# Performance work log

Measured on AMD Instinct MI355X. Metric: run time of the kernel, lower is better.

## Reference

```python
import jax, jax.numpy as jnp
import numpy as np

EPS = 0.5
MIN_SAMPLES = 5


def setup_inputs() -> dict:
    key = jax.random.key(0)
    X = jax.random.uniform(key, (12288, 8), dtype=jnp.float32)
    return {"X": X}


def reference(X):
    """DBSCAN: eps-range queries + cluster expansion, expressed as
    eps-graph connected components over core points (same clustering
    as the serial BFS in the original module; cluster ids are assigned
    in order of each cluster's minimum core index, matching the
    ascending-scan discovery order of the original)."""
    N = X.shape[0]
    SENTINEL = jnp.int32(N)

    # pairwise squared Euclidean distances [N, N] (KDTree range query equivalent)
    sq = jnp.sum(X * X, axis=1)
    d2 = sq[:, None] + sq[None, :] - 2.0 * (X @ X.T)
    adj = d2 <= (EPS * EPS)                      # eps-neighborhood (includes self)

    density = jnp.sum(adj, axis=1)               # |query_ball_point(x_i, eps)|
    core = density >= MIN_SAMPLES                # core-point mask

    # core-core edges: BFS expansion only propagates through cores
    core_adj = adj & core[None, :] & core[:, None]

    idx = jnp.arange(N, dtype=jnp.int32)
    init = jnp.where(core, idx, SENTINEL)        # each core starts as its own root

    def prop(lbl):
        # min label over core neighbors (min-plus propagation = connected components)
        nb_min = jnp.min(jnp.where(core_adj, lbl[None, :], SENTINEL), axis=1)
        return jnp.minimum(lbl, nb_min)

    def cond(state):
        cur, prev = state
        return jnp.any(cur != prev)

    def body(state):
        cur, _ = state
        return prop(cur), cur

    lbl, _ = jax.lax.while_loop(cond, body, (prop(init), init))

    # border points: non-core points within eps of a core join that core's cluster
    core_nb = jnp.min(jnp.where(adj & core[None, :], lbl[None, :], SENTINEL), axis=1)
    root = jnp.where(core, lbl, core_nb)         # SENTINEL -> noise

    # compact cluster ids: rank of each cluster root (min core index) ascending,
    # matching the original's sequential discovery order k = 0, 1, ...
    is_root = core & (lbl == idx)
    rank = jnp.cumsum(is_root.astype(jnp.int32)) - 1   # rank[i] valid where is_root[i]
    labels = jnp.where(root < SENTINEL,
                       rank[jnp.clip(root, 0, N - 1)],
                       jnp.int32(-1))
    return labels
```

## Files before the change

kernel.cpp:

```cpp
#include <hip/hip_runtime.h>

#define NPTS 12288
#define DIMS 8
#define EPS2 0.25f
#define MINS 5
#define NIB1 (NPTS / 256)
#define NW   (NPTS / 32)
#define SENT NPTS
#define RMAX 512
#define W    (RMAX / 32)
#define BIGL 0x3fffffff
#define FT   128
#define FB   256
#define FBGRID 256
#define HB   96
#define HT   512

#define ATHR 256
#define AROWS 2
#define ATI  (ATHR * AROWS)
#define ANIB (NPTS / ATI)
#define ANJB 48
#define AJC  (NPTS / ANJB)
#define AWCH (AJC / 32)

typedef float v2f __attribute__((ext_vector_type(2)));

__device__ __forceinline__ float dot8(const v2f* xi, const float4& a, const float4& b) {
  v2f y0 = {a.x, a.y}, y1 = {a.z, a.w}, y2 = {b.x, b.y}, y3 = {b.z, b.w};
  v2f d = xi[0] * y0;
  d = __builtin_elementwise_fma(xi[1], y1, d);
  d = __builtin_elementwise_fma(xi[2], y2, d);
  d = __builtin_elementwise_fma(xi[3], y3, d);
  return d.x + d.y;
}


__global__ __launch_bounds__(ATHR) void k_adj(const float* __restrict__ X,
                                              unsigned int* __restrict__ adj,
                                              int* __restrict__ density) {
  __shared__ float4 xs[AJC][2];
  __shared__ float sqs[AJC];
  int t = threadIdx.x;
  int j0 = blockIdx.y * AJC;
  {
    int j = j0 + t;
    float4 a = ((const float4*)X)[j * 2];
    float4 b = ((const float4*)X)[j * 2 + 1];
    xs[t][0] = a; xs[t][1] = b;
    float sv = 0.f;
    sv = fmaf(a.x, a.x, sv); sv = fmaf(a.y, a.y, sv); sv = fmaf(a.z, a.z, sv); sv = fmaf(a.w, a.w, sv);
    sv = fmaf(b.x, b.x, sv); sv = fmaf(b.y, b.y, sv); sv = fmaf(b.z, b.z, sv); sv = fmaf(b.w, b.w, sv);
    sqs[t] = sv;
  }
  int i0 = blockIdx.x * ATI + t, i1 = i0 + ATHR;
  v2f xi0[4], xi1[4];
  {
    float4 a0 = ((const float4*)X)[i0 * 2], b0v = ((const float4*)X)[i0 * 2 + 1];
    float4 a1 = ((const float4*)X)[i1 * 2], b1v = ((const float4*)X)[i1 * 2 + 1];
    xi0[0] = (v2f){a0.x, a0.y}; xi0[1] = (v2f){a0.z, a0.w};
    xi0[2] = (v2f){b0v.x, b0v.y}; xi0[3] = (v2f){b0v.z, b0v.w};
    xi1[0] = (v2f){a1.x, a1.y}; xi1[1] = (v2f){a1.z, a1.w};
    xi1[2] = (v2f){b1v.x, b1v.y}; xi1[3] = (v2f){b1v.z, b1v.w};
  }
  float sq0 = 0.f, sq1 = 0.f;
#pragma unroll
  for (int q = 0; q < 4; q++) {
    v2f p0 = xi0[q] * xi0[q], p1 = xi1[q] * xi1[q];
    sq0 += p0.x + p0.y; sq1 += p1.x + p1.y;
  }
  __syncthreads();
  unsigned int acc0[AWCH], acc1[AWCH];
#pragma unroll
  for (int w = 0; w < AWCH; w++) {
    unsigned int b0 = 0u, b1 = 0u;
#pragma unroll 4
    for (int bit = 0; bit < 32; bit++) {
      int jj = (w << 5) + bit;
      float4 xa = xs[jj][0], xb = xs[jj][1];
      float sj = sqs[jj];
      unsigned int m = 1u << bit;
      float d20 = (sq0 + sj) - 2.0f * dot8(xi0, xa, xb);
      float d21 = (sq1 + sj) - 2.0f * dot8(xi1, xa, xb);
      if (d20 <= EPS2) b0 |= m;
      if (d21 <= EPS2) b1 |= m;
    }
    acc0[w] = b0; acc1[w] = b1;
  }
  uint4* dst0 = (uint4*)(adj + (size_t)i0 * NW + blockIdx.y * AWCH);
  uint4* dst1 = (uint4*)(adj + (size_t)i1 * NW + blockIdx.y * AWCH);
  dst0[0] = make_uint4(acc0[0], acc0[1], acc0[2], acc0[3]);
  dst0[1] = make_uint4(acc0[4], acc0[5], acc0[6], acc0[7]);
  dst1[0] = make_uint4(acc1[0], acc1[1], acc1[2], acc1[3]);
  dst1[1] = make_uint4(acc1[4], acc1[5], acc1[6], acc1[7]);
  int pc0 = 0, pc1 = 0;
#pragma unroll
  for (int w = 0; w < AWCH; w++) { pc0 += __popc(acc0[w]); pc1 += __popc(acc1[w]); }
  atomicAdd(&density[i0], pc0);
  atomicAdd(&density[i1], pc1);
}

__global__ __launch_bounds__(HT) void k_hook2(const unsigned int* __restrict__ adj,
                                              const int* __restrict__ density,
                                              unsigned long long* __restrict__ corebm,
                                              int* __restrict__ hook) {
  __shared__ unsigned long long cb64[NW / 2];
  const unsigned int* cb = (const unsigned int*)cb64;
  int t = threadIdx.x;
  for (int base = 0; base < NPTS; base += HT) {
    int i = base + t;
    unsigned long long m = __ballot(density[i] >= MINS);
    if ((t & 63) == 0) cb64[i >> 6] = m;
  }
  __syncthreads();
  if (blockIdx.x == 0) {
    for (int w = t; w < NW / 2; w += HT) corebm[w] = cb64[w];
  }
  int lane = t & 63, wv = t >> 6;
  int gw = blockIdx.x * (HT / 64) + wv;
  for (int i = gw; i < NPTS; i += (HT / 64) * HB) {
    const unsigned int* row = adj + (size_t)i * NW;
    int wi = i >> 5;
    int m = i;
    for (int w = lane; w <= wi; w += 64) {
      unsigned int x = row[w] & cb[w];
      if (w == wi) x &= (1u << (i & 31)) - 1;
      if (x) m = min(m, (w << 5) + __ffs(x) - 1);
    }
#pragma unroll
    for (int off = 32; off >= 1; off >>= 1) m = min(m, __shfl_xor(m, off, 64));
    if (lane == 0) hook[i] = m;
  }
}

__global__ __launch_bounds__(1024) void k_rid(const int* __restrict__ density,
                                              const int* __restrict__ hook,
                                              int* __restrict__ Rptr,
                                              int* __restrict__ labL,
                                              int* __restrict__ bcount) {
  __shared__ unsigned short ridS[NPTS];
  __shared__ int wsum[16];
  int t = threadIdx.x;
  int lane = t & 63, wid = t >> 6;
  const int SEG = NPTS / 1024;
  int base = t * SEG;
  int flags = 0;
  int s = 0;
#pragma unroll
  for (int k = 0; k < SEG; k++) {
    int i = base + k;
    int f = (density[i] >= MINS && hook[i] == i) ? 1 : 0;
    flags |= f << k;
    s += f;
  }
  int segsum = s;
#pragma unroll
  for (int off = 1; off < 64; off <<= 1) {
    int n = __shfl_up(s, off, 64);
    if (lane >= off) s += n;
  }
  if (lane == 63) wsum[wid] = s;
  __syncthreads();
  int woff = 0;
  for (int w = 0; w < wid; w++) woff += wsum[w];
  int run = woff + s - segsum;
#pragma unroll
  for (int k = 0; k < SEG; k++) {
    ridS[base + k] = (unsigned short)run;
    run += (flags >> k) & 1;
  }
  if (t == 1023) *Rptr = run;
  if (t == 0) *bcount = 0;
  __syncthreads();
  for (int k = 0; k < SEG; k++) {
    int i = base + k;
    int lab = -1;
    if (density[i] >= MINS) {
      int v = i, h = hook[v];
      while (h != v) { v = h; h = hook[v]; }
      lab = min((int)ridS[v], RMAX - 1);
    }
    labL[i] = lab;
  }
}

__global__ __launch_bounds__(FB) void k_fillbm(const unsigned int* __restrict__ adj,
                                               const unsigned int* __restrict__ cb32,
                                               const int* __restrict__ labL,
                                               unsigned int* __restrict__ bm) {
  __shared__ unsigned int bmL[RMAX * W];
  __shared__ unsigned short labS[NPTS];
  __shared__ unsigned int cb[NW];
  int t = threadIdx.x;
  for (int q = t; q < RMAX * W; q += FB) bmL[q] = 0u;
  for (int q = t; q < NPTS; q += FB) labS[q] = (unsigned short)(labL[q] + 1);
  for (int w = t; w < NW; w += FB) cb[w] = cb32[w];
  __syncthreads();
  int lane = t & 63, wv = t >> 6;
  int gw = blockIdx.x * 4 + wv;
  for (int i = gw; i < NPTS; i += 4 * FBGRID) {
    int a0 = (int)labS[i] - 1;
    if (a0 < 0) continue;
    const unsigned int* row = adj + (size_t)i * NW;
    int wi = i >> 5;
    for (int w = wi + lane; w < NW; w += 64) {
      unsigned int x = row[w] & cb[w];
      if (w == wi) x &= (0xFFFFFFFEu << (i & 31));
      while (x) {
        int b = __ffs(x) - 1; x &= x - 1;
        int lj = (int)labS[(w << 5) + b] - 1;
        if (lj != a0) {
          atomicOr(&bmL[a0 * W + (lj >> 5)], 1u << (lj & 31));
          atomicOr(&bmL[lj * W + (a0 >> 5)], 1u << (a0 & 31));
        }
      }
    }
  }
  __syncthreads();
  for (int q = t; q < RMAX * W; q += FB) {
    unsigned int v = bmL[q];
    if (v) atomicOr(&bm[q], v);
  }
}

__global__ __launch_bounds__(RMAX) void k_cc(const unsigned int* __restrict__ bm,
                                             const int* __restrict__ Rptr,
                                             const int* __restrict__ labL,
                                             int* __restrict__ labArr,
                                             int* __restrict__ blist,
                                             int* __restrict__ bcount,
                                             float* __restrict__ out) {
  __shared__ int lbl[RMAX];
  __shared__ int mn[RMAX];
  __shared__ int chg, cmp;
  int a = threadIdx.x;
  int R = *Rptr; if (R > RMAX) R = RMAX;
  lbl[a] = a;
  __syncthreads();
  while (true) {
    int m = lbl[a];
    if (a < R) {
      const unsigned int* row = bm + a * W;
#pragma unroll
      for (int w = 0; w < W; w++) {
        unsigned int bits = row[w];
        while (bits) {
          int b = __ffs(bits) - 1;
          bits &= bits - 1;
          m = min(m, lbl[(w << 5) + b]);
        }
      }
    }
    mn[a] = m;
    if (a == 0) chg = 0;
    __syncthreads();
    int l = lbl[a];
    if (m < l) { atomicMin(&lbl[l], m); atomicMin(&lbl[a], m); chg = 1; }
    __syncthreads();
    while (true) {
      if (a == 0) cmp = 0;
      __syncthreads();
      int nl = lbl[lbl[a]];
      __syncthreads();
      if (nl < lbl[a]) { lbl[a] = nl; cmp = 1; }
      __syncthreads();
      if (!cmp) break;
    }
    if (!chg) break;
    __syncthreads();
  }
  int flag = (a < R && lbl[a] == a) ? 1 : 0;
  mn[a] = flag;
  __syncthreads();
  for (int off = 1; off < RMAX; off <<= 1) {
    int v = mn[a];
    int add = (a >= off) ? mn[a - off] : 0;
    __syncthreads();
    mn[a] = v + add;
    __syncthreads();
  }
  int myclab = mn[lbl[a]] - 1;
  mn[a] = myclab;
  __syncthreads();
  for (int base = 0; base < NPTS; base += RMAX) {
    int i = base + a;
    int l = labL[i];
    if (l >= 0) {
      int lab = mn[l];
      labArr[i] = lab;
      out[i] = (float)lab;
    } else {
      labArr[i] = BIGL;
      out[i] = -1.0f;
      int pos = atomicAdd(bcount, 1);
      blist[pos] = i;
    }
  }
}

__global__ __launch_bounds__(FT) void k_border(const unsigned int* __restrict__ adj,
                                               const unsigned int* __restrict__ cb32,
                                               const int* __restrict__ labArr,
                                               const int* __restrict__ blist,
                                               const int* __restrict__ bcount,
                                               float* __restrict__ out) {
  __shared__ unsigned int cb[NW];
  __shared__ int wm[FT / 64];
  int t = threadIdx.x;
  for (int w = t; w < NW; w += FT) cb[w] = cb32[w];
  __syncthreads();
  int count = *bcount;
  for (int k = blockIdx.x; k < count; k += gridDim.x) {
    int p = blist[k];
    const unsigned int* row = adj + (size_t)p * NW;
    int m = BIGL;
    for (int w = t; w < NW; w += FT) {
      unsigned int x = row[w] & cb[w];
      while (x) {
        int b = __ffs(x) - 1; x &= x - 1;
        m = min(m, labArr[(w << 5) + b]);
      }
    }
#pragma unroll
    for (int off = 32; off >= 1; off >>= 1) m = min(m, __shfl_xor(m, off, 64));
    if ((t & 63) == 0) wm[t >> 6] = m;
    __syncthreads();
    if (t == 0) {
      int mm = min(wm[0], wm[1]);
      out[p] = (mm < BIGL) ? (float)mm : -1.0f;
    }
    __syncthreads();
  }
}


extern "C" void kernel_launch(void* const* d_in, const int* in_sizes, int n_in,
                              void* d_out, int out_size, void* d_ws, size_t ws_size,
                              hipStream_t stream) {
  const float* X = (const float*)d_in[0];
  float* out = (float*)d_out;

  char* ws = (char*)d_ws;
  unsigned int* adj = (unsigned int*)ws;
  size_t off = (size_t)NPTS * NW * 4;
  int* density = (int*)(ws + off);           off += 4 * NPTS;
  int* hook    = (int*)(ws + off);           off += 4 * NPTS;
  int* labL    = (int*)(ws + off);           off += 4 * NPTS;
  int* labArr  = (int*)(ws + off);           off += 4 * NPTS;
  int* blist   = (int*)(ws + off);           off += 4 * NPTS;
  unsigned long long* corebm = (unsigned long long*)(ws + off); off += 2048;
  unsigned int* bm  = (unsigned int*)(ws + off); off += 4 * RMAX * W;
  int* Rptr    = (int*)(ws + off);
  int* bcount  = Rptr + 1;

  hipMemsetAsync(density, 0, 4 * NPTS, stream);
  hipMemsetAsync(bm, 0, 4 * RMAX * W, stream);

  dim3 gridA(ANIB, ANJB);

  k_adj<<<gridA, ATHR, 0, stream>>>(X, adj, density);
  k_hook2<<<HB, HT, 0, stream>>>(adj, density, corebm, hook);
  k_rid<<<1, 1024, 0, stream>>>(density, hook, Rptr, labL, bcount);
  k_fillbm<<<FBGRID, FB, 0, stream>>>(adj, (const unsigned int*)corebm, labL, bm);
  k_cc<<<1, RMAX, 0, stream>>>(bm, Rptr, labL, labArr, blist, bcount, out);
  k_border<<<256, FT, 0, stream>>>(adj, (const unsigned int*)corebm, labArr, blist, bcount, out);
}
```

Before: 241.5 us.

## Fuse post-adjacency stages into one persistent kernel with software grid barriers

Replaces the five kernels after the adjacency build (hook, root id, bitmap fill, component merge, border assignment) with a single persistent 256-block kernel that separates phases with an atomic generation-counter grid barrier. Density is now computed from adjacency rows inside that kernel instead of with atomics in k_adj, and the two memsets shrink to one tiny control reset. The goal is to remove the launch gaps and tail idle time between many small kernels. In exchange, correctness depends on all 256 blocks being co-resident, and the single-block phases leave the rest of the grid spinning at barriers.

```diff
diff --git a/kernel.cpp b/kernel.cpp
--- a/kernel.cpp
+++ b/kernel.cpp
@@ -4,21 +4,17 @@
 #define DIMS 8
 #define EPS2 0.25f
 #define MINS 5
-#define NIB1 (NPTS / 256)
 #define NW   (NPTS / 32)
-#define SENT NPTS
 #define RMAX 512
 #define W    (RMAX / 32)
 #define BIGL 0x3fffffff
-#define FT   128
-#define FB   256
-#define FBGRID 256
-#define HB   96
-#define HT   512
+
+#define MB   256
+#define MT   512
+#define MW   (MB * MT / 64)
 
 #define ATHR 256
-#define AROWS 2
-#define ATI  (ATHR * AROWS)
+#define ATI  512
 #define ANIB (NPTS / ATI)
 #define ANJB 48
 #define AJC  (NPTS / ANJB)
@@ -35,10 +31,8 @@
   return d.x + d.y;
 }
 
-
 __global__ __launch_bounds__(ATHR) void k_adj(const float* __restrict__ X,
-                                              unsigned int* __restrict__ adj,
-                                              int* __restrict__ density) {
+                                              unsigned int* __restrict__ adj) {
   __shared__ float4 xs[AJC][2];
   __shared__ float sqs[AJC];
   int t = threadIdx.x;
@@ -93,243 +87,252 @@
   dst0[1] = make_uint4(acc0[4], acc0[5], acc0[6], acc0[7]);
   dst1[0] = make_uint4(acc1[0], acc1[1], acc1[2], acc1[3]);
   dst1[1] = make_uint4(acc1[4], acc1[5], acc1[6], acc1[7]);
-  int pc0 = 0, pc1 = 0;
-#pragma unroll
-  for (int w = 0; w < AWCH; w++) { pc0 += __popc(acc0[w]); pc1 += __popc(acc1[w]); }
-  atomicAdd(&density[i0], pc0);
-  atomicAdd(&density[i1], pc1);
-}
-
-__global__ __launch_bounds__(HT) void k_hook2(const unsigned int* __restrict__ adj,
-                                              const int* __restrict__ density,
-                                              unsigned long long* __restrict__ corebm,
-                                              int* __restrict__ hook) {
-  __shared__ unsigned long long cb64[NW / 2];
-  const unsigned int* cb = (const unsigned int*)cb64;
+}
+
+__device__ __forceinline__ void gridbar(int* cnt, int* gen, int t) {
+  __syncthreads();
+  __threadfence();
+  if (t == 0) {
+    int g = __hip_atomic_load(gen, __ATOMIC_RELAXED, __HIP_MEMORY_SCOPE_AGENT);
+    int v = __hip_atomic_fetch_add(cnt, 1, __ATOMIC_ACQ_REL, __HIP_MEMORY_SCOPE_AGENT);
+    if (v == MB - 1) {
+      __hip_atomic_store(cnt, 0, __ATOMIC_RELAXED, __HIP_MEMORY_SCOPE_AGENT);
+      __hip_atomic_fetch_add(gen, 1, __ATOMIC_ACQ_REL, __HIP_MEMORY_SCOPE_AGENT);
+    } else {
+      while (__hip_atomic_load(gen, __ATOMIC_ACQUIRE, __HIP_MEMORY_SCOPE_AGENT) == g)
+        __builtin_amdgcn_s_sleep(8);
+    }
+  }
+  __syncthreads();
+}
+
+__global__ __launch_bounds__(MT) void k_mega(const unsigned int* __restrict__ adj,
+                                             int* __restrict__ density,
+                                             int* __restrict__ hook,
+                                             int* __restrict__ labL,
+                                             int* __restrict__ labArr,
+                                             int* __restrict__ blist,
+                                             unsigned int* __restrict__ bm,
+                                             int* __restrict__ clabG,
+                                             int* __restrict__ Rptr,
+                                             int* __restrict__ cnt,
+                                             int* __restrict__ gen,
+                                             int* __restrict__ bcount,
+                                             float* __restrict__ out) {
+  __shared__ unsigned long long cb64S[NW / 2];
+  __shared__ unsigned int big[RMAX * W + NPTS / 2];
+  __shared__ int wsum[MT / 64];
+  __shared__ int chg, cmp;
+  unsigned int* cbS = (unsigned int*)cb64S;
   int t = threadIdx.x;
-  for (int base = 0; base < NPTS; base += HT) {
+  int lane = t & 63, wv = t >> 6;
+  int gw = blockIdx.x * (MT / 64) + wv;
+
+  if (blockIdx.x == 0)
+    for (int q = t; q < RMAX * W; q += MT) bm[q] = 0u;
+  for (int i = gw; i < NPTS; i += MW) {
+    const uint4* row = (const uint4*)(adj + (size_t)i * NW);
+    uint4 v = row[lane];
+    int s = __popc(v.x) + __popc(v.y) + __popc(v.z) + __popc(v.w);
+    if (lane < NW / 4 - 64) {
+      uint4 v2 = row[64 + lane];
+      s += __popc(v2.x) + __popc(v2.y) + __popc(v2.z) + __popc(v2.w);
+    }
+#pragma unroll
+    for (int off = 32; off >= 1; off >>= 1) s += __shfl_xor(s, off, 64);
+    if (lane == 0) density[i] = s;
+  }
+  gridbar(cnt, gen, t);
+
+  for (int base = 0; base < NPTS; base += MT) {
     int i = base + t;
     unsigned long long m = __ballot(density[i] >= MINS);
-    if ((t & 63) == 0) cb64[i >> 6] = m;
+    if ((t & 63) == 0) cb64S[i >> 6] = m;
   }
   __syncthreads();
-  if (blockIdx.x == 0) {
-    for (int w = t; w < NW / 2; w += HT) corebm[w] = cb64[w];
-  }
-  int lane = t & 63, wv = t >> 6;
-  int gw = blockIdx.x * (HT / 64) + wv;
-  for (int i = gw; i < NPTS; i += (HT / 64) * HB) {
+  for (int i = gw; i < NPTS; i += MW) {
     const unsigned int* row = adj + (size_t)i * NW;
     int wi = i >> 5;
     int m = i;
     for (int w = lane; w <= wi; w += 64) {
-      unsigned int x = row[w] & cb[w];
-      if (w == wi) x &= (1u << (i & 31)) - 1;
+      unsigned int x = row[w] & cbS[w];
+      if (w == wi) x &= (1u << (i & 31)) - 1u;
       if (x) m = min(m, (w << 5) + __ffs(x) - 1);
     }
 #pragma unroll
     for (int off = 32; off >= 1; off >>= 1) m = min(m, __shfl_xor(m, off, 64));
     if (lane == 0) hook[i] = m;
   }
-}
-
-__global__ __launch_bounds__(1024) void k_rid(const int* __restrict__ density,
-                                              const int* __restrict__ hook,
-                                              int* __restrict__ Rptr,
-                                              int* __restrict__ labL,
-                                              int* __restrict__ bcount) {
-  __shared__ unsigned short ridS[NPTS];
-  __shared__ int wsum[16];
-  int t = threadIdx.x;
-  int lane = t & 63, wid = t >> 6;
-  const int SEG = NPTS / 1024;
-  int base = t * SEG;
-  int flags = 0;
-  int s = 0;
-#pragma unroll
-  for (int k = 0; k < SEG; k++) {
-    int i = base + k;
-    int f = (density[i] >= MINS && hook[i] == i) ? 1 : 0;
-    flags |= f << k;
-    s += f;
-  }
-  int segsum = s;
-#pragma unroll
-  for (int off = 1; off < 64; off <<= 1) {
-    int n = __shfl_up(s, off, 64);
-    if (lane >= off) s += n;
-  }
-  if (lane == 63) wsum[wid] = s;
-  __syncthreads();
-  int woff = 0;
-  for (int w = 0; w < wid; w++) woff += wsum[w];
-  int run = woff + s - segsum;
-#pragma unroll
-  for (int k = 0; k < SEG; k++) {
-    ridS[base + k] = (unsigned short)run;
-    run += (flags >> k) & 1;
-  }
-  if (t == 1023) *Rptr = run;
-  if (t == 0) *bcount = 0;
-  __syncthreads();
-  for (int k = 0; k < SEG; k++) {
-    int i = base + k;
-    int lab = -1;
-    if (density[i] >= MINS) {
-      int v = i, h = hook[v];
-      while (h != v) { v = h; h = hook[v]; }
-      lab = min((int)ridS[v], RMAX - 1);
-    }
-    labL[i] = lab;
-  }
-}
-
-__global__ __launch_bounds__(FB) void k_fillbm(const unsigned int* __restrict__ adj,
-                                               const unsigned int* __restrict__ cb32,
-                                               const int* __restrict__ labL,
-                                               unsigned int* __restrict__ bm) {
-  __shared__ unsigned int bmL[RMAX * W];
-  __shared__ unsigned short labS[NPTS];
-  __shared__ unsigned int cb[NW];
-  int t = threadIdx.x;
-  for (int q = t; q < RMAX * W; q += FB) bmL[q] = 0u;
-  for (int q = t; q < NPTS; q += FB) labS[q] = (unsigned short)(labL[q] + 1);
-  for (int w = t; w < NW; w += FB) cb[w] = cb32[w];
-  __syncthreads();
-  int lane = t & 63, wv = t >> 6;
-  int gw = blockIdx.x * 4 + wv;
-  for (int i = gw; i < NPTS; i += 4 * FBGRID) {
-    int a0 = (int)labS[i] - 1;
-    if (a0 < 0) continue;
-    const unsigned int* row = adj + (size_t)i * NW;
-    int wi = i >> 5;
-    for (int w = wi + lane; w < NW; w += 64) {
-      unsigned int x = row[w] & cb[w];
-      if (w == wi) x &= (0xFFFFFFFEu << (i & 31));
-      while (x) {
-        int b = __ffs(x) - 1; x &= x - 1;
-        int lj = (int)labS[(w << 5) + b] - 1;
-        if (lj != a0) {
-          atomicOr(&bmL[a0 * W + (lj >> 5)], 1u << (lj & 31));
-          atomicOr(&bmL[lj * W + (a0 >> 5)], 1u << (a0 & 31));
+  gridbar(cnt, gen, t);
+
+  if (blockIdx.x == 0) {
+    unsigned short* ridS = (unsigned short*)big;
+    const int SEG = NPTS / MT;
+    int base = t * SEG;
+    int flags = 0, s = 0;
+    for (int k = 0; k < SEG; k++) {
+      int i = base + k;
+      int f = (density[i] >= MINS && hook[i] == i) ? 1 : 0;
+      flags |= f << k;
+      s += f;
+    }
+    int segsum = s;
+#pragma unroll
+    for (int off = 1; off < 64; off <<= 1) {
+      int n = __shfl_up(s, off, 64);
+      if (lane >= off) s += n;
+    }
+    if (lane == 63) wsum[wv] = s;
+    __syncthreads();
+    int woff = 0;
+    for (int w = 0; w < wv; w++) woff += wsum[w];
+    int run = woff + s - segsum;
+    for (int k = 0; k < SEG; k++) {
+      ridS[base + k] = (unsigned short)run;
+      run += (flags >> k) & 1;
+    }
+    if (t == MT - 1) *Rptr = run;
+    __syncthreads();
+    for (int k = 0; k < SEG; k++) {
+      int i = base + k;
+      int lab = -1;
+      if (density[i] >= MINS) {
+        int v = i, h = hook[v];
+        while (h != v) { v = h; h = hook[v]; }
+        lab = min((int)ridS[v], RMAX - 1);
+      }
+      labL[i] = lab;
+    }
+  }
+  gridbar(cnt, gen, t);
+
+  {
+    unsigned int* bmL = big;
+    unsigned short* labS = (unsigned short*)(big + RMAX * W);
+    for (int q = t; q < RMAX * W; q += MT) bmL[q] = 0u;
+    for (int q = t; q < NPTS; q += MT) labS[q] = (unsigned short)(labL[q] + 1);
+    __syncthreads();
+    for (int i = gw; i < NPTS; i += MW) {
+      int a0 = (int)labS[i] - 1;
+      if (a0 < 0) continue;
+      const unsigned int* row = adj + (size_t)i * NW;
+      int wi = i >> 5;
+      for (int w = wi + lane; w < NW; w += 64) {
+        unsigned int x = row[w] & cbS[w];
+        if (w == wi) x &= (0xFFFFFFFEu << (i & 31));
+        while (x) {
+          int b = __ffs(x) - 1; x &= x - 1;
+          int lj = (int)labS[(w << 5) + b] - 1;
+          if (lj != a0) {
+            atomicOr(&bmL[a0 * W + (lj >> 5)], 1u << (lj & 31));
+            atomicOr(&bmL[lj * W + (a0 >> 5)], 1u << (a0 & 31));
+          }
         }
       }
     }
-  }
-  __syncthreads();
-  for (int q = t; q < RMAX * W; q += FB) {
-    unsigned int v = bmL[q];
-    if (v) atomicOr(&bm[q], v);
-  }
-}
-
-__global__ __launch_bounds__(RMAX) void k_cc(const unsigned int* __restrict__ bm,
-                                             const int* __restrict__ Rptr,
-                                             const int* __restrict__ labL,
-                                             int* __restrict__ labArr,
-                                             int* __restrict__ blist,
-                                             int* __restrict__ bcount,
-                                             float* __restrict__ out) {
-  __shared__ int lbl[RMAX];
-  __shared__ int mn[RMAX];
-  __shared__ int chg, cmp;
-  int a = threadIdx.x;
-  int R = *Rptr; if (R > RMAX) R = RMAX;
-  lbl[a] = a;
-  __syncthreads();
-  while (true) {
-    int m = lbl[a];
-    if (a < R) {
-      const unsigned int* row = bm + a * W;
-#pragma unroll
-      for (int w = 0; w < W; w++) {
-        unsigned int bits = row[w];
-        while (bits) {
-          int b = __ffs(bits) - 1;
-          bits &= bits - 1;
-          m = min(m, lbl[(w << 5) + b]);
+    __syncthreads();
+    for (int q = t; q < RMAX * W; q += MT) {
+      unsigned int v = bmL[q];
+      if (v) atomicOr(&bm[q], v);
+    }
+  }
+  gridbar(cnt, gen, t);
+
+  if (blockIdx.x == 0) {
+    int* lbl = (int*)big;
+    int* mn = lbl + RMAX;
+    int a = t;
+    int R = *Rptr; if (R > RMAX) R = RMAX;
+    lbl[a] = a;
+    __syncthreads();
+    while (true) {
+      int m = lbl[a];
+      if (a < R) {
+        const unsigned int* row = bm + a * W;
+#pragma unroll
+        for (int w = 0; w < W; w++) {
+          unsigned int bits = row[w];
+          while (bits) {
+            int b = __ffs(bits) - 1;
+            bits &= bits - 1;
+            m = min(m, lbl[(w << 5) + b]);
+          }
         }
       }
-    }
-    mn[a] = m;
-    if (a == 0) chg = 0;
-    __syncthreads();
-    int l = lbl[a];
-    if (m < l) { atomicMin(&lbl[l], m); atomicMin(&lbl[a], m); chg = 1; }
-    __syncthreads();
-    while (true) {
-      if (a == 0) cmp = 0;
-      __syncthreads();
-      int nl = lbl[lbl[a]];
-      __syncthreads();
-      if (nl < lbl[a]) { lbl[a] = nl; cmp = 1; }
-      __syncthreads();
-      if (!cmp) break;
-    }
-    if (!chg) break;
-    __syncthreads();
-  }
-  int flag = (a < R && lbl[a] == a) ? 1 : 0;
-  mn[a] = flag;
-  __syncthreads();
-  for (int off = 1; off < RMAX; off <<= 1) {
-    int v = mn[a];
-    int add = (a >= off) ? mn[a - off] : 0;
-    __syncthreads();
-    mn[a] = v + add;
-    __syncthreads();
-  }
-  int myclab = mn[lbl[a]] - 1;
-  mn[a] = myclab;
-  __syncthreads();
-  for (int base = 0; base < NPTS; base += RMAX) {
-    int i = base + a;
-    int l = labL[i];
-    if (l >= 0) {
-      int lab = mn[l];
-      labArr[i] = lab;
-      out[i] = (float)lab;
-    } else {
-      labArr[i] = BIGL;
-      out[i] = -1.0f;
-      int pos = atomicAdd(bcount, 1);
-      blist[pos] = i;
-    }
-  }
-}
-
-__global__ __launch_bounds__(FT) void k_border(const unsigned int* __restrict__ adj,
-                                               const unsigned int* __restrict__ cb32,
-                                               const int* __restrict__ labArr,
-                                               const int* __restrict__ blist,
-                                               const int* __restrict__ bcount,
-                                               float* __restrict__ out) {
-  __shared__ unsigned int cb[NW];
-  __shared__ int wm[FT / 64];
-  int t = threadIdx.x;
-  for (int w = t; w < NW; w += FT) cb[w] = cb32[w];
-  __syncthreads();
-  int count = *bcount;
-  for (int k = blockIdx.x; k < count; k += gridDim.x) {
-    int p = blist[k];
-    const unsigned int* row = adj + (size_t)p * NW;
-    int m = BIGL;
-    for (int w = t; w < NW; w += FT) {
-      unsigned int x = row[w] & cb[w];
-      while (x) {
-        int b = __ffs(x) - 1; x &= x - 1;
-        m = min(m, labArr[(w << 5) + b]);
-      }
-    }
-#pragma unroll
-    for (int off = 32; off >= 1; off >>= 1) m = min(m, __shfl_xor(m, off, 64));
-    if ((t & 63) == 0) wm[t >> 6] = m;
-    __syncthreads();
-    if (t == 0) {
-      int mm = min(wm[0], wm[1]);
-      out[p] = (mm < BIGL) ? (float)mm : -1.0f;
-    }
-    __syncthreads();
+      mn[a] = m;
+      if (a == 0) chg = 0;
+      __syncthreads();
+      int l = lbl[a];
+      if (m < l) { atomicMin(&lbl[l], m); atomicMin(&lbl[a], m); chg = 1; }
+      __syncthreads();
+      while (true) {
+        if (a == 0) cmp = 0;
+        __syncthreads();
+        int nl = lbl[lbl[a]];
+        __syncthreads();
+        if (nl < lbl[a]) { lbl[a] = nl; cmp = 1; }
+        __syncthreads();
+        if (!cmp) break;
+      }
+      if (!chg) break;
+      __syncthreads();
+    }
+    int flag = (a < R && lbl[a] == a) ? 1 : 0;
+    mn[a] = flag;
+    __syncthreads();
+    for (int off = 1; off < RMAX; off <<= 1) {
+      int v = mn[a];
+      int add = (a >= off) ? mn[a - off] : 0;
+      __syncthreads();
+      mn[a] = v + add;
+      __syncthreads();
+    }
+    clabG[a] = mn[lbl[a]] - 1;
+  }
+  gridbar(cnt, gen, t);
+
+  {
+    int gid = blockIdx.x * MT + t;
+    if (gid < NPTS) {
+      int l = labL[gid];
+      if (l >= 0) {
+        int lab = clabG[l];
+        labArr[gid] = lab;
+        out[gid] = (float)lab;
+      } else {
+        labArr[gid] = BIGL;
+        out[gid] = -1.0f;
+        int pos = atomicAdd(bcount, 1);
+        blist[pos] = gid;
+      }
+    }
+  }
+  gridbar(cnt, gen, t);
+
+  {
+    int count = *bcount;
+    for (int k = blockIdx.x; k < count; k += MB) {
+      int p = blist[k];
+      const unsigned int* row = adj + (size_t)p * NW;
+      int m = BIGL;
+      if (t < NW) {
+        unsigned int x = row[t] & cbS[t];
+        while (x) {
+          int b = __ffs(x) - 1; x &= x - 1;
+          m = min(m, labArr[(t << 5) + b]);
+        }
+      }
+#pragma unroll
+      for (int off = 32; off >= 1; off >>= 1) m = min(m, __shfl_xor(m, off, 64));
+      if (lane == 0) wsum[wv] = m;
+      __syncthreads();
+      if (t == 0) {
+        int mm = wsum[0];
+        for (int w = 1; w < MT / 64; w++) mm = min(mm, wsum[w]);
+        out[p] = (mm < BIGL) ? (float)mm : -1.0f;
+      }
+      __syncthreads();
+    }
   }
 }
 
@@ -348,20 +351,17 @@
   int* labL    = (int*)(ws + off);           off += 4 * NPTS;
   int* labArr  = (int*)(ws + off);           off += 4 * NPTS;
   int* blist   = (int*)(ws + off);           off += 4 * NPTS;
-  unsigned long long* corebm = (unsigned long long*)(ws + off); off += 2048;
-  unsigned int* bm  = (unsigned int*)(ws + off); off += 4 * RMAX * W;
-  int* Rptr    = (int*)(ws + off);
-  int* bcount  = Rptr + 1;
-
-  hipMemsetAsync(density, 0, 4 * NPTS, stream);
-  hipMemsetAsync(bm, 0, 4 * RMAX * W, stream);
+  unsigned int* bm = (unsigned int*)(ws + off); off += 4 * RMAX * W;
+  int* clabG   = (int*)(ws + off);           off += 4 * RMAX;
+  int* Rptr    = (int*)(ws + off);           off += 4;
+  int* ctrl    = (int*)(ws + off);
+  int* cnt = ctrl, *gen = ctrl + 1, *bcount = ctrl + 2;
+
+  hipMemsetAsync(ctrl, 0, 12, stream);
 
   dim3 gridA(ANIB, ANJB);
 
-  k_adj<<<gridA, ATHR, 0, stream>>>(X, adj, density);
-  k_hook2<<<HB, HT, 0, stream>>>(adj, density, corebm, hook);
-  k_rid<<<1, 1024, 0, stream>>>(density, hook, Rptr, labL, bcount);
-  k_fillbm<<<FBGRID, FB, 0, stream>>>(adj, (const unsigned int*)corebm, labL, bm);
-  k_cc<<<1, RMAX, 0, stream>>>(bm, Rptr, labL, labArr, blist, bcount, out);
-  k_border<<<256, FT, 0, stream>>>(adj, (const unsigned int*)corebm, labArr, blist, bcount, out);
-}
+  k_adj<<<gridA, ATHR, 0, stream>>>(X, adj);
+  k_mega<<<MB, MT, 0, stream>>>(adj, density, hook, labL, labArr, blist,
+                                bm, clabG, Rptr, cnt, gen, bcount, out);
+}
```

Measured after the change: 885.8 us. +266.8%, slower.
